# Kernel optimization log

Measured on AMD Instinct MI355X. Metric: run time of the kernel, lower is better.

## Reference

```python
import math
import jax, jax.numpy as jnp
import numpy as np

HEAD_DIM = 128
NUM_HEADS = 16
ROPE_BASE = 10000.0


def _rope_tables(seq_len, dim, dtype):
    inv_freq = 1.0 / (ROPE_BASE ** (jnp.arange(0, dim, 2, dtype=jnp.float32) / dim))
    t = jnp.arange(seq_len, dtype=jnp.float32)
    freqs = jnp.einsum('i,j->ij', t, inv_freq)          # [S, D/2]
    emb = jnp.concatenate([freqs, freqs], axis=-1)       # [S, D]
    return jnp.cos(emb).astype(dtype), jnp.sin(emb).astype(dtype)


def _rotate_half(x):
    x1, x2 = jnp.split(x, 2, axis=-1)
    return jnp.concatenate([-x2, x1], axis=-1)


def _apply_rope(x, cos, sin):
    # x: [B, S, H, D]; cos/sin: [S, D] broadcast over batch and heads
    return x * cos[None, :, None, :] + _rotate_half(x) * sin[None, :, None, :]


def setup_inputs() -> dict:
    key = jax.random.key(0)
    k1, k2, k3 = jax.random.split(key, 3)
    B, S, dim = 2, 2048, 2048
    out_dim = (NUM_HEADS + 2 * NUM_HEADS) * HEAD_DIM  # kvph=1 -> 3*H*D = 6144
    x = jax.random.normal(k1, (B, S, dim), dtype=jnp.float32)
    w_qkv = jax.random.normal(k2, (out_dim, dim), dtype=jnp.float32) * 0.02
    w_out = jax.random.normal(k3, (dim, NUM_HEADS * HEAD_DIM), dtype=jnp.float32) * 0.02
    return {"x": x, "w_qkv": w_qkv, "w_out": w_out}


def reference(x, w_qkv, w_out):
    B, S, _ = x.shape
    H, D = NUM_HEADS, HEAD_DIM
    qkv = jnp.einsum('bsd,od->bso', x, w_qkv)            # [B, S, 3*H*D]
    qkv = qkv.reshape(B, S, 3 * H, D)
    q = qkv[:, :, :H, :]                                 # [B, S, H, D]
    k = qkv[:, :, H:2 * H, :]
    v = qkv[:, :, 2 * H:, :]
    cos, sin = _rope_tables(S, D, x.dtype)
    q = _apply_rope(q, cos, sin)
    k = _apply_rope(k, cos, sin)
    scale = 1.0 / math.sqrt(D)
    logits = jnp.einsum('bqhd,bkhd->bhqk', q, k) * scale  # [B, H, S, S]
    attn = jax.nn.softmax(logits.astype(jnp.float32), axis=-1).astype(logits.dtype)
    out = jnp.einsum('bhqk,bkhd->bqhd', attn, v)          # [B, S, H, D]
    out = out.reshape(B, S, H * D)
    return jnp.einsum('bso,do->bsd', out, w_out)
```

## Files before the change

kernel.cpp:

```cpp
#include <hip/hip_runtime.h>
#include <math.h>
#include <stdint.h>

typedef unsigned short u16;
typedef unsigned int u32;
typedef float f32x4 __attribute__((ext_vector_type(4)));
typedef __bf16 bf16x8 __attribute__((ext_vector_type(8)));

typedef const __attribute__((address_space(1))) u32* gas1;
typedef __attribute__((address_space(3))) u32* las3;

#define B_ 2
#define S_ 2048
#define DM_ 2048
#define H_ 16
#define HD_ 128
#define NO_ 6144
#define M_ 4096

__device__ __forceinline__ u16 f2bf(float f) {
  u32 u = __float_as_uint(f);
  u32 r = (u + 0x7fffu + ((u >> 16) & 1u)) >> 16;
  return (u16)r;
}
__device__ __forceinline__ float bf2f(u16 h) {
  return __uint_as_float(((u32)h) << 16);
}

__global__ void prep_all(const float* __restrict__ x, const float* __restrict__ wqkv,
                         const float* __restrict__ wout, u16* __restrict__ xbf,
                         u16* __restrict__ wqkvb, u16* __restrict__ woutb,
                         float* __restrict__ ct, float* __restrict__ st) {
  const int C1 = (M_ * DM_) / 4, C2 = (NO_ * DM_) / 4, C3 = (DM_ * DM_) / 4;
  const int C4 = S_ * 64;
  const int total = C1 + C2 + C3 + C4;
  for (int i = blockIdx.x * blockDim.x + threadIdx.x; i < total;
       i += gridDim.x * blockDim.x) {
    if (i < C1 + C2 + C3) {
      const float* in;
      u16* out;
      int k;
      if (i < C1) {
        in = x; out = xbf; k = i;
      } else if (i < C1 + C2) {
        in = wqkv; out = wqkvb; k = i - C1;
      } else {
        in = wout; out = woutb; k = i - C1 - C2;
      }
      float4 v = *(const float4*)(in + (size_t)k * 4);
      ushort4 o;
      o.x = f2bf(v.x); o.y = f2bf(v.y); o.z = f2bf(v.z); o.w = f2bf(v.w);
      *(ushort4*)(out + (size_t)k * 4) = o;
    } else {
      int k = i - (C1 + C2 + C3);
      int s = k >> 6, j = k & 63;
      float inv = powf(10000.0f, -(float)j / 64.0f);
      float f = (float)s * inv;
      ct[k] = cosf(f);
      st[k] = sinf(f);
    }
  }
}

__global__ __launch_bounds__(512, 2) void gemm8_bt(const u16* __restrict__ A,
                                                   const u16* __restrict__ B,
                                                   u16* __restrict__ C,
                                                   int M, int N, int K, int ldc) {
  __shared__ u16 lds8[2][2][2][8192];
  const int t = threadIdx.x;
  const int w = t >> 6, l = t & 63, lr = l & 15, lg = l >> 4;
  const int wm = w >> 2, wn = w & 3;
  const int m0 = blockIdx.y * 256, n0 = blockIdx.x * 256;
  const int r0 = t >> 2;
  const int c = (t & 3) ^ ((t >> 3) & 3);
  const int swr = (lr >> 1) & 3;
  const u16* pA0 = A + (size_t)(m0 + r0) * K + c * 8;
  const u16* pB0 = B + (size_t)(n0 + r0) * K + c * 8;
  const size_t j1 = (size_t)128 * K;

  f32x4 acc[8][4] = {};
  bf16x8 af[8], bq[4];

  const int NT = K / 64, NI = NT / 2;

#define STG(T_, kh_, op_, buf_)                                                      \
  do {                                                                               \
    const u16* s_ = (op_ ? pB0 : pA0) + (T_) * 64 + (kh_) * 32;                      \
    u16* d_ = &lds8[buf_][op_][kh_][0] + w * 512;                                    \
    __builtin_amdgcn_global_load_lds((gas1)s_, (las3)d_, 16, 0, 0);                  \
    __builtin_amdgcn_global_load_lds((gas1)(s_ + j1), (las3)(d_ + 4096), 16, 0, 0);  \
  } while (0)

#define LDF(buf_, kh_)                                                            \
  do {                                                                            \
    const u16* a_ = &lds8[buf_][0][kh_][0];                                       \
    const u16* b_ = &lds8[buf_][1][kh_][0];                                       \
    _Pragma("unroll") for (int mi = 0; mi < 8; ++mi)                              \
        af[mi] = *(const bf16x8*)&a_[(wm * 128 + mi * 16 + lr) * 32 +             \
                                     ((lg ^ swr) * 8)];                           \
    _Pragma("unroll") for (int ni = 0; ni < 4; ++ni)                              \
        bq[ni] = *(const bf16x8*)&b_[(wn * 64 + ni * 16 + lr) * 32 +              \
                                     ((lg ^ swr) * 8)];                           \
  } while (0)

#define MFH(h_)                                                                \
  do {                                                                         \
    __builtin_amdgcn_s_setprio(1);                                             \
    _Pragma("unroll") for (int mi = 0; mi < 4; ++mi)                           \
        _Pragma("unroll") for (int ni = 0; ni < 4; ++ni)                       \
            acc[(h_) * 4 + mi][ni] = __builtin_amdgcn_mfma_f32_16x16x32_bf16(  \
                af[(h_) * 4 + mi], bq[ni], acc[(h_) * 4 + mi][ni], 0, 0, 0);   \
    __builtin_amdgcn_s_setprio(0);                                             \
  } while (0)

#define BAR() __builtin_amdgcn_s_barrier()
#define LGKM0() asm volatile("s_waitcnt lgkmcnt(0)" ::: "memory")
#define VM6() asm volatile("s_waitcnt vmcnt(6)" ::: "memory")

  STG(0, 0, 0, 0); STG(0, 0, 1, 0); STG(0, 1, 0, 0); STG(0, 1, 1, 0);
  STG(1, 0, 0, 1); STG(1, 0, 1, 1); STG(1, 1, 0, 1);
  VM6();
  BAR();

  for (int i = 0; i < NI; ++i) {
    const int T = 2 * i;
    const int Tp2 = (T + 2 < NT) ? T + 2 : NT - 1;
    const int Tp3 = (T + 3 < NT) ? T + 3 : NT - 1;
    LDF(0, 0);
    STG(T + 1, 1, 1, 1);
    BAR(); LGKM0(); MFH(0); BAR();
    STG(Tp2, 0, 0, 0);
    BAR(); MFH(1); BAR();
    LDF(0, 1);
    STG(Tp2, 0, 1, 0);
    BAR(); LGKM0(); MFH(0); BAR();
    STG(Tp2, 1, 0, 0);
    VM6(); BAR(); MFH(1); BAR();
    LDF(1, 0);
    STG(Tp2, 1, 1, 0);
    BAR(); LGKM0(); MFH(0); BAR();
    STG(Tp3, 0, 0, 1);
    BAR(); MFH(1); BAR();
    LDF(1, 1);
    STG(Tp3, 0, 1, 1);
    BAR(); LGKM0(); MFH(0); BAR();
    STG(Tp3, 1, 0, 1);
    VM6(); BAR(); MFH(1); BAR();
  }
  asm volatile("s_waitcnt vmcnt(0)" ::: "memory");
  BAR();

#pragma unroll
  for (int mi = 0; mi < 8; ++mi)
#pragma unroll
    for (int ni = 0; ni < 4; ++ni) {
      int row = m0 + wm * 128 + mi * 16 + lg * 4;
      int col = n0 + wn * 64 + ni * 16 + lr;
#pragma unroll
      for (int j = 0; j < 4; ++j)
        C[(size_t)(row + j) * ldc + col] = f2bf(acc[mi][ni][j]);
    }
#undef STG
#undef LDF
#undef MFH
#undef BAR
#undef LGKM0
#undef VM6
}

template <int OUT_BF16>
__global__ __launch_bounds__(256) void gemm_bt(const u16* __restrict__ A,
                                               const u16* __restrict__ B,
                                               void* __restrict__ Cv,
                                               int M, int N, int K, int ldc) {
  __shared__ u16 lA[128 * 32];
  __shared__ u16 lB[128 * 32];
  const int t = threadIdx.x;
  const int m0 = blockIdx.y * 128, n0 = blockIdx.x * 128;
  const int w = t >> 6, l = t & 63, lr = l & 15, lg = l >> 4;
  const int wm = (w >> 1) * 64, wn = (w & 1) * 64;
  f32x4 acc[4][4] = {};
  const int srow = t >> 2;
  const int scol = ((t & 3) ^ ((t >> 3) & 3)) * 8;
  const int swr = (lr >> 1) & 3;
  const u16* Ag = A + (size_t)(m0 + srow) * K + scol;
  const u16* Bg = B + (size_t)(n0 + srow) * K + scol;

  for (int k0 = 0; k0 < K; k0 += 32) {
    __syncthreads();
#pragma unroll
    for (int i = 0; i < 2; i++) {
      __builtin_amdgcn_global_load_lds((gas1)(Ag + (size_t)i * 64 * K + k0),
                                       (las3)(lA + (i * 256 + w * 64) * 8), 16, 0, 0);
      __builtin_amdgcn_global_load_lds((gas1)(Bg + (size_t)i * 64 * K + k0),
                                       (las3)(lB + (i * 256 + w * 64) * 8), 16, 0, 0);
    }
    __syncthreads();
    bf16x8 af[4], bfr[4];
#pragma unroll
    for (int mi = 0; mi < 4; mi++)
      af[mi] = *(const bf16x8*)&lA[(wm + mi * 16 + lr) * 32 + (lg ^ swr) * 8];
#pragma unroll
    for (int ni = 0; ni < 4; ni++)
      bfr[ni] = *(const bf16x8*)&lB[(wn + ni * 16 + lr) * 32 + (lg ^ swr) * 8];
#pragma unroll
    for (int mi = 0; mi < 4; mi++)
#pragma unroll
      for (int ni = 0; ni < 4; ni++)
        acc[mi][ni] =
            __builtin_amdgcn_mfma_f32_16x16x32_bf16(af[mi], bfr[ni], acc[mi][ni], 0, 0, 0);
  }

#pragma unroll
  for (int mi = 0; mi < 4; mi++)
#pragma unroll
    for (int ni = 0; ni < 4; ni++) {
      int row = m0 + wm + mi * 16 + lg * 4;
      int col = n0 + wn + ni * 16 + lr;
      if (OUT_BF16) {
        u16* C = (u16*)Cv;
#pragma unroll
        for (int j = 0; j < 4; j++) C[(size_t)(row + j) * ldc + col] = f2bf(acc[mi][ni][j]);
      } else {
        float* C = (float*)Cv;
#pragma unroll
        for (int j = 0; j < 4; j++) C[(size_t)(row + j) * ldc + col] = acc[mi][ni][j];
      }
    }
}

__global__ void rope_apply(u16* __restrict__ qkv, const float* __restrict__ ct,
                           const float* __restrict__ st) {
  int i = blockIdx.x * blockDim.x + threadIdx.x;
  int j = (i & 31) * 2;
  int hh = (i >> 5) & 31;
  int row = i >> 10;
  int s = row & (S_ - 1);
  int col = (hh < 16) ? hh * 128 : 2048 + (hh - 16) * 128;
  u16* p = qkv + (size_t)row * NO_ + col + j;
  u32 a = *(const u32*)&p[0];
  u32 bm = *(const u32*)&p[64];
  float2 cc = *(const float2*)&ct[(s << 6) + j];
  float2 ss = *(const float2*)&st[(s << 6) + j];
  float e10 = bf2f((u16)a), e11 = bf2f((u16)(a >> 16));
  float e20 = bf2f((u16)bm), e21 = bf2f((u16)(bm >> 16));
  float o10 = e10 * cc.x - e20 * ss.x;
  float o11 = e11 * cc.y - e21 * ss.y;
  float o20 = e20 * cc.x + e10 * ss.x;
  float o21 = e21 * cc.y + e11 * ss.y;
  if (hh < 16) {
    const float kq = 0.08838834764831845f * 1.4426950408889634f;
    o10 *= kq; o11 *= kq; o20 *= kq; o21 *= kq;
  }
  *(u32*)&p[0] = (u32)f2bf(o10) | ((u32)f2bf(o11) << 16);
  *(u32*)&p[64] = (u32)f2bf(o20) | ((u32)f2bf(o21) << 16);
}

__global__ __launch_bounds__(256) void transpose_v(const u16* __restrict__ qkv,
                                                   u16* __restrict__ vt) {
  __shared__ u16 lds[128 * 64];
  const int bh = blockIdx.y;
  const int b = bh >> 4, h = bh & 15;
  const int s0 = blockIdx.x * 64;
  const int t = threadIdx.x;
  union { uint4 v; u16 e[8]; } uu;
#pragma unroll
  for (int i = 0; i < 4; i++) {
    int s = i * 16 + (t >> 4);
    int dc = (t & 15) * 8;
    uu.v = *(const uint4*)(qkv + (size_t)(b * S_ + s0 + s) * NO_ + 4096 + h * 128 + dc);
#pragma unroll
    for (int q = 0; q < 8; q++) {
      int d = dc + q;
      lds[d * 64 + (s ^ (((d >> 3) & 7) << 3))] = uu.e[q];
    }
  }
  __syncthreads();
#pragma unroll
  for (int i = 0; i < 4; i++) {
    int d = i * 32 + (t >> 3);
    int sc = (t & 7) * 8;
    uint4 v = *(const uint4*)&lds[d * 64 + (sc ^ (((d >> 3) & 7) << 3))];
    *(uint4*)(vt + (size_t)(bh * 128 + d) * S_ + s0 + sc) = v;
  }
}

__global__ __launch_bounds__(256, 2) void flash_attn(const u16* __restrict__ qkv,
                                                     const u16* __restrict__ vt,
                                                     u16* __restrict__ ao) {
  __shared__ u16 lK[2][64 * 128];
  __shared__ u16 lV[2][128 * 64];
  __shared__ u16 lP[4][2][16 * 64];
  const int t = threadIdx.x;
  const int w = t >> 6, l = t & 63, lr = l & 15, lg = l >> 4;
  const int bid = blockIdx.y * gridDim.x + blockIdx.x;
  const int xcd = bid & 7, v = bid >> 3;
  const int bh = xcd + 8 * (v >> 4);
  const int q0 = (v & 15) * 128;
  const int b = bh >> 4, h = bh & 15;

  bf16x8 qf[2][4];
#pragma unroll
  for (int g = 0; g < 2; g++) {
    const u16* Qg = qkv + (size_t)(b * S_ + q0 + w * 32 + g * 16 + lr) * NO_ + h * 128;
#pragma unroll
    for (int c = 0; c < 4; c++) qf[g][c] = *(const bf16x8*)(Qg + c * 32 + lg * 8);
  }

  f32x4 acc[2][8] = {};
  float l_run[2] = {0.f, 0.f};

  const u16* ksrc[4];
  const u16* vsrc[4];
#pragma unroll
  for (int q = 0; q < 4; q++) {
    int rt = w * 16 + q * 4 + (l >> 4);
    int ck = (l & 15) ^ (rt & 15);
    ksrc[q] = qkv + (size_t)(b * S_ + rt) * NO_ + 2048 + h * 128 + ck * 8;
    int d = w * 32 + q * 8 + (l >> 3);
    int cv = (l & 7) ^ (d & 7);
    vsrc[q] = vt + (size_t)(bh * 128 + d) * S_ + cv * 8;
  }

#pragma unroll
  for (int q = 0; q < 4; q++) {
    __builtin_amdgcn_global_load_lds((gas1)ksrc[q],
                                     (las3)(lK[0] + (w * 16 + q * 4) * 128), 16, 0, 0);
    __builtin_amdgcn_global_load_lds((gas1)vsrc[q],
                                     (las3)(lV[0] + (w * 32 + q * 8) * 64), 16, 0, 0);
    ksrc[q] += (size_t)64 * NO_;
    vsrc[q] += 64;
  }
  __syncthreads();

  const int NT = S_ / 64;
  for (int kt = 0; kt < NT; kt++) {
    const int cur = kt & 1;
    if (kt + 1 < NT) {
#pragma unroll
      for (int q = 0; q < 4; q++) {
        __builtin_amdgcn_global_load_lds((gas1)ksrc[q],
                                         (las3)(lK[cur ^ 1] + (w * 16 + q * 4) * 128), 16, 0, 0);
        __builtin_amdgcn_global_load_lds((gas1)vsrc[q],
                                         (las3)(lV[cur ^ 1] + (w * 32 + q * 8) * 64), 16, 0, 0);
        ksrc[q] += (size_t)64 * NO_;
        vsrc[q] += 64;
      }
    }

    f32x4 sc[2][4];
#pragma unroll
    for (int g = 0; g < 2; g++)
#pragma unroll
      for (int cb = 0; cb < 4; cb++) sc[g][cb] = (f32x4){0.f, 0.f, 0.f, 0.f};
    __builtin_amdgcn_s_setprio(1);
#pragma unroll
    for (int cb = 0; cb < 4; cb++) {
      int r = cb * 16 + lr;
#pragma unroll
      for (int c = 0; c < 4; c++) {
        bf16x8 kf = *(const bf16x8*)&lK[cur][r * 128 + ((c * 32 + lg * 8) ^ ((r & 15) << 3))];
        sc[0][cb] = __builtin_amdgcn_mfma_f32_16x16x32_bf16(kf, qf[0][c], sc[0][cb], 0, 0, 0);
        sc[1][cb] = __builtin_amdgcn_mfma_f32_16x16x32_bf16(kf, qf[1][c], sc[1][cb], 0, 0, 0);
      }
    }
    __builtin_amdgcn_s_setprio(0);

#pragma unroll
    for (int g = 0; g < 2; g++) {
      float ps = 0.f;
#pragma unroll
      for (int cb = 0; cb < 4; cb++)
#pragma unroll
        for (int j = 0; j < 4; j++) {
          float p = exp2f(sc[g][cb][j]);
          sc[g][cb][j] = p;
          ps += p;
        }
      l_run[g] += ps;
    }

#pragma unroll
    for (int g = 0; g < 2; g++) {
      u16* lPw = lP[w][g];
#pragma unroll
      for (int cb = 0; cb < 4; cb++) {
        u32 p01, p23;
        asm("v_cvt_pk_bf16_f32 %0, %1, %2" : "=v"(p01) : "v"(sc[g][cb][0]), "v"(sc[g][cb][1]));
        asm("v_cvt_pk_bf16_f32 %0, %1, %2" : "=v"(p23) : "v"(sc[g][cb][2]), "v"(sc[g][cb][3]));
        uint2 pk;
        pk.x = p01;
        pk.y = p23;
        *(uint2*)&lPw[lr * 64 + ((cb * 16 + lg * 4) ^ ((lr & 7) << 3))] = pk;
      }
    }

    __builtin_amdgcn_s_setprio(1);
#pragma unroll
    for (int c2 = 0; c2 < 2; c2++) {
      bf16x8 pf0 = *(const bf16x8*)&lP[w][0][lr * 64 + ((c2 * 32 + lg * 8) ^ ((lr & 7) << 3))];
      bf16x8 pf1 = *(const bf16x8*)&lP[w][1][lr * 64 + ((c2 * 32 + lg * 8) ^ ((lr & 7) << 3))];
#pragma unroll
      for (int nb = 0; nb < 8; nb++) {
        int r = nb * 16 + lr;
        bf16x8 vf = *(const bf16x8*)&lV[cur][r * 64 + ((c2 * 32 + lg * 8) ^ ((r & 7) << 3))];
        acc[0][nb] = __builtin_amdgcn_mfma_f32_16x16x32_bf16(pf0, vf, acc[0][nb], 0, 0, 0);
        acc[1][nb] = __builtin_amdgcn_mfma_f32_16x16x32_bf16(pf1, vf, acc[1][nb], 0, 0, 0);
      }
    }
    __builtin_amdgcn_s_setprio(0);

    __syncthreads();
  }

#pragma unroll
  for (int g = 0; g < 2; g++) {
    float lsum = l_run[g];
    lsum += __shfl_xor(lsum, 16);
    lsum += __shfl_xor(lsum, 32);
    float linv[4];
#pragma unroll
    for (int j = 0; j < 4; j++) linv[j] = 1.0f / __shfl(lsum, lg * 4 + j);
#pragma unroll
    for (int nb = 0; nb < 8; nb++)
#pragma unroll
      for (int j = 0; j < 4; j++) {
        int qrow = q0 + w * 32 + g * 16 + lg * 4 + j;
        ao[(size_t)(b * S_ + qrow) * 2048 + h * 128 + nb * 16 + lr] =
            f2bf(acc[g][nb][j] * linv[j]);
      }
  }
}

extern "C" void kernel_launch(void* const* d_in, const int* in_sizes, int n_in,
                              void* d_out, int out_size, void* d_ws, size_t ws_size,
                              hipStream_t stream) {
  const float* x = (const float*)d_in[0];
  const float* wqkv = (const float*)d_in[1];
  const float* wout = (const float*)d_in[2];
  float* out = (float*)d_out;

  char* ws = (char*)d_ws;
  u16* xbf = (u16*)(ws);
  u16* wqkvb = (u16*)(ws + ((size_t)16 << 20));
  u16* woutb = (u16*)(ws + ((size_t)40 << 20));
  u16* qkv = (u16*)(ws + ((size_t)48 << 20));
  u16* vtb = (u16*)(ws + ((size_t)96 << 20));
  float* ct = (float*)(ws + ((size_t)112 << 20));
  float* st = (float*)(ws + ((size_t)112 << 20) + ((size_t)1 << 19));
  u16* aout = xbf;

  prep_all<<<2048, 256, 0, stream>>>(x, wqkv, wout, xbf, wqkvb, woutb, ct, st);
  gemm8_bt<<<dim3(16, 16), 512, 0, stream>>>(xbf, wqkvb, qkv, M_, 4096, DM_, NO_);
  gemm_bt<1><<<dim3(16, 32), 256, 0, stream>>>(
      xbf, wqkvb + (size_t)4096 * DM_, qkv + 4096, M_, 2048, DM_, NO_);
  rope_apply<<<(M_ * 32 * 32) / 256, 256, 0, stream>>>(qkv, ct, st);
  transpose_v<<<dim3(S_ / 64, B_ * H_), 256, 0, stream>>>(qkv, vtb);
  flash_attn<<<dim3(16, 32), 256, 0, stream>>>(qkv, vtb, aout);
  gemm_bt<0><<<dim3(DM_ / 128, M_ / 128), 256, 0, stream>>>(aout, woutb, out, M_, DM_, DM_,
                                                            DM_);
}
```

Baseline: 305.8 us.

## Fuse RoPE into QK GEMM epilogue and V transpose into V GEMM

Applies rotary embedding and the Q scale directly in the QK GEMM epilogue. Each wave swaps its accumulator tile with its partner wave (the other half of the head dim) through LDS, and reads transposed cos/sin tables. The V projection GEMM now writes V transposed through an LDS staging tile. This removes the separate rope_apply and transpose_v kernels along with their extra global reads and writes of qkv. In exchange, the epilogues carry extra LDS traffic, a barrier and strided table loads, and the partner pairing relies on the tile layout mapping half-dims to adjacent waves.

```diff
diff --git a/kernel.cpp b/kernel.cpp
--- a/kernel.cpp
+++ b/kernel.cpp
@@ -30,9 +30,9 @@
 __global__ void prep_all(const float* __restrict__ x, const float* __restrict__ wqkv,
                          const float* __restrict__ wout, u16* __restrict__ xbf,
                          u16* __restrict__ wqkvb, u16* __restrict__ woutb,
-                         float* __restrict__ ct, float* __restrict__ st) {
+                         float* __restrict__ ctT, float* __restrict__ stT) {
   const int C1 = (M_ * DM_) / 4, C2 = (NO_ * DM_) / 4, C3 = (DM_ * DM_) / 4;
-  const int C4 = S_ * 64;
+  const int C4 = 64 * S_;
   const int total = C1 + C2 + C3 + C4;
   for (int i = blockIdx.x * blockDim.x + threadIdx.x; i < total;
        i += gridDim.x * blockDim.x) {
@@ -53,11 +53,11 @@
       *(ushort4*)(out + (size_t)k * 4) = o;
     } else {
       int k = i - (C1 + C2 + C3);
-      int s = k >> 6, j = k & 63;
+      int j = k >> 11, s = k & 2047;
       float inv = powf(10000.0f, -(float)j / 64.0f);
       float f = (float)s * inv;
-      ct[k] = cosf(f);
-      st[k] = sinf(f);
+      ctT[k] = cosf(f);
+      stT[k] = sinf(f);
     }
   }
 }
@@ -65,7 +65,9 @@
 __global__ __launch_bounds__(512, 2) void gemm8_bt(const u16* __restrict__ A,
                                                    const u16* __restrict__ B,
                                                    u16* __restrict__ C,
-                                                   int M, int N, int K, int ldc) {
+                                                   int M, int N, int K, int ldc,
+                                                   const float* __restrict__ ctT,
+                                                   const float* __restrict__ stT) {
   __shared__ u16 lds8[2][2][2][8192];
   const int t = threadIdx.x;
   const int w = t >> 6, l = t & 63, lr = l & 15, lg = l >> 4;
@@ -150,16 +152,49 @@
   asm volatile("s_waitcnt vmcnt(0)" ::: "memory");
   BAR();
 
+  u16* xb = (u16*)lds8;
 #pragma unroll
   for (int mi = 0; mi < 8; ++mi)
 #pragma unroll
     for (int ni = 0; ni < 4; ++ni) {
-      int row = m0 + wm * 128 + mi * 16 + lg * 4;
+      ushort4 pk;
+      pk.x = f2bf(acc[mi][ni][0]);
+      pk.y = f2bf(acc[mi][ni][1]);
+      pk.z = f2bf(acc[mi][ni][2]);
+      pk.w = f2bf(acc[mi][ni][3]);
+      int li = (l * 4) ^ ((l >> 4) << 3);
+      *(ushort4*)&xb[(w * 32 + mi * 4 + ni) * 256 + li] = pk;
+    }
+  __syncthreads();
+  const int wp = w ^ 1;
+  const int pos = w & 1;
+  const bool isQ = (n0 < 2048);
+  const float kq = 0.08838834764831845f * 1.4426950408889634f;
+#pragma unroll
+  for (int mi = 0; mi < 8; ++mi) {
+    int row = m0 + wm * 128 + mi * 16 + lg * 4;
+    int s0 = row & (S_ - 1);
+#pragma unroll
+    for (int ni = 0; ni < 4; ++ni) {
+      int li = (l * 4) ^ ((l >> 4) << 3);
+      ushort4 pp = *(const ushort4*)&xb[(wp * 32 + mi * 4 + ni) * 256 + li];
+      int j0 = ni * 16 + lr;
+      float4 c4 = *(const float4*)&ctT[j0 * S_ + s0];
+      float4 s4 = *(const float4*)&stT[j0 * S_ + s0];
       int col = n0 + wn * 64 + ni * 16 + lr;
-#pragma unroll
-      for (int j = 0; j < 4; ++j)
-        C[(size_t)(row + j) * ldc + col] = f2bf(acc[mi][ni][j]);
-    }
+      const u16 pe[4] = {pp.x, pp.y, pp.z, pp.w};
+      const float cc[4] = {c4.x, c4.y, c4.z, c4.w};
+      const float sv[4] = {s4.x, s4.y, s4.z, s4.w};
+#pragma unroll
+      for (int j = 0; j < 4; ++j) {
+        float own = acc[mi][ni][j];
+        float part = bf2f(pe[j]);
+        float o = pos ? own * cc[j] + part * sv[j] : own * cc[j] - part * sv[j];
+        if (isQ) o *= kq;
+        C[(size_t)(row + j) * ldc + col] = f2bf(o);
+      }
+    }
+  }
 #undef STG
 #undef LDF
 #undef MFH
@@ -168,7 +203,7 @@
 #undef VM6
 }
 
-template <int OUT_BF16>
+template <int MODE>
 __global__ __launch_bounds__(256) void gemm_bt(const u16* __restrict__ A,
                                                const u16* __restrict__ B,
                                                void* __restrict__ Cv,
@@ -211,77 +246,52 @@
             __builtin_amdgcn_mfma_f32_16x16x32_bf16(af[mi], bfr[ni], acc[mi][ni], 0, 0, 0);
   }
 
-#pragma unroll
-  for (int mi = 0; mi < 4; mi++)
-#pragma unroll
-    for (int ni = 0; ni < 4; ni++) {
-      int row = m0 + wm + mi * 16 + lg * 4;
-      int col = n0 + wn + ni * 16 + lr;
-      if (OUT_BF16) {
-        u16* C = (u16*)Cv;
-#pragma unroll
-        for (int j = 0; j < 4; j++) C[(size_t)(row + j) * ldc + col] = f2bf(acc[mi][ni][j]);
-      } else {
-        float* C = (float*)Cv;
-#pragma unroll
-        for (int j = 0; j < 4; j++) C[(size_t)(row + j) * ldc + col] = acc[mi][ni][j];
-      }
-    }
-}
-
-__global__ void rope_apply(u16* __restrict__ qkv, const float* __restrict__ ct,
-                           const float* __restrict__ st) {
-  int i = blockIdx.x * blockDim.x + threadIdx.x;
-  int j = (i & 31) * 2;
-  int hh = (i >> 5) & 31;
-  int row = i >> 10;
-  int s = row & (S_ - 1);
-  int col = (hh < 16) ? hh * 128 : 2048 + (hh - 16) * 128;
-  u16* p = qkv + (size_t)row * NO_ + col + j;
-  u32 a = *(const u32*)&p[0];
-  u32 bm = *(const u32*)&p[64];
-  float2 cc = *(const float2*)&ct[(s << 6) + j];
-  float2 ss = *(const float2*)&st[(s << 6) + j];
-  float e10 = bf2f((u16)a), e11 = bf2f((u16)(a >> 16));
-  float e20 = bf2f((u16)bm), e21 = bf2f((u16)(bm >> 16));
-  float o10 = e10 * cc.x - e20 * ss.x;
-  float o11 = e11 * cc.y - e21 * ss.y;
-  float o20 = e20 * cc.x + e10 * ss.x;
-  float o21 = e21 * cc.y + e11 * ss.y;
-  if (hh < 16) {
-    const float kq = 0.08838834764831845f * 1.4426950408889634f;
-    o10 *= kq; o11 *= kq; o20 *= kq; o21 *= kq;
-  }
-  *(u32*)&p[0] = (u32)f2bf(o10) | ((u32)f2bf(o11) << 16);
-  *(u32*)&p[64] = (u32)f2bf(o20) | ((u32)f2bf(o21) << 16);
-}
-
-__global__ __launch_bounds__(256) void transpose_v(const u16* __restrict__ qkv,
-                                                   u16* __restrict__ vt) {
-  __shared__ u16 lds[128 * 64];
-  const int bh = blockIdx.y;
-  const int b = bh >> 4, h = bh & 15;
-  const int s0 = blockIdx.x * 64;
-  const int t = threadIdx.x;
-  union { uint4 v; u16 e[8]; } uu;
-#pragma unroll
-  for (int i = 0; i < 4; i++) {
-    int s = i * 16 + (t >> 4);
-    int dc = (t & 15) * 8;
-    uu.v = *(const uint4*)(qkv + (size_t)(b * S_ + s0 + s) * NO_ + 4096 + h * 128 + dc);
-#pragma unroll
-    for (int q = 0; q < 8; q++) {
-      int d = dc + q;
-      lds[d * 64 + (s ^ (((d >> 3) & 7) << 3))] = uu.e[q];
-    }
-  }
-  __syncthreads();
-#pragma unroll
-  for (int i = 0; i < 4; i++) {
-    int d = i * 32 + (t >> 3);
-    int sc = (t & 7) * 8;
-    uint4 v = *(const uint4*)&lds[d * 64 + (sc ^ (((d >> 3) & 7) << 3))];
-    *(uint4*)(vt + (size_t)(bh * 128 + d) * S_ + s0 + sc) = v;
+  if constexpr (MODE == 2) {
+    __shared__ u16 tbuf[128 * 128];
+#pragma unroll
+    for (int mi = 0; mi < 4; mi++)
+#pragma unroll
+      for (int ni = 0; ni < 4; ni++) {
+        int r0 = wm + mi * 16 + lg * 4;
+        int d = wn + ni * 16 + lr;
+        ushort4 pk;
+        pk.x = f2bf(acc[mi][ni][0]);
+        pk.y = f2bf(acc[mi][ni][1]);
+        pk.z = f2bf(acc[mi][ni][2]);
+        pk.w = f2bf(acc[mi][ni][3]);
+        *(ushort4*)&tbuf[d * 128 + (r0 ^ ((d & 7) << 3))] = pk;
+      }
+    __syncthreads();
+    const int h = n0 >> 7;
+    const int b = m0 >> 11;
+    const int s0 = m0 & (S_ - 1);
+    u16* vt = (u16*)Cv;
+#pragma unroll
+    for (int i = 0; i < 8; i++) {
+      int d = i * 16 + (t >> 4);
+      int sc = (t & 15) * 8;
+      uint4 vv = *(const uint4*)&tbuf[d * 128 + (sc ^ ((d & 7) << 3))];
+      *(uint4*)&vt[(size_t)((b * 16 + h) * 128 + d) * S_ + s0 + sc] = vv;
+    }
+  } else {
+#pragma unroll
+    for (int mi = 0; mi < 4; mi++)
+#pragma unroll
+      for (int ni = 0; ni < 4; ni++) {
+        int row = m0 + wm + mi * 16 + lg * 4;
+        int col = n0 + wn + ni * 16 + lr;
+        if (MODE == 1) {
+          u16* C = (u16*)Cv;
+#pragma unroll
+          for (int j = 0; j < 4; j++)
+            C[(size_t)(row + j) * ldc + col] = f2bf(acc[mi][ni][j]);
+        } else {
+          float* C = (float*)Cv;
+#pragma unroll
+          for (int j = 0; j < 4; j++)
+            C[(size_t)(row + j) * ldc + col] = acc[mi][ni][j];
+        }
+      }
   }
 }
 
@@ -446,16 +456,15 @@
   u16* woutb = (u16*)(ws + ((size_t)40 << 20));
   u16* qkv = (u16*)(ws + ((size_t)48 << 20));
   u16* vtb = (u16*)(ws + ((size_t)96 << 20));
-  float* ct = (float*)(ws + ((size_t)112 << 20));
-  float* st = (float*)(ws + ((size_t)112 << 20) + ((size_t)1 << 19));
+  float* ctT = (float*)(ws + ((size_t)112 << 20));
+  float* stT = (float*)(ws + ((size_t)112 << 20) + ((size_t)1 << 19));
   u16* aout = xbf;
 
-  prep_all<<<2048, 256, 0, stream>>>(x, wqkv, wout, xbf, wqkvb, woutb, ct, st);
-  gemm8_bt<<<dim3(16, 16), 512, 0, stream>>>(xbf, wqkvb, qkv, M_, 4096, DM_, NO_);
-  gemm_bt<1><<<dim3(16, 32), 256, 0, stream>>>(
-      xbf, wqkvb + (size_t)4096 * DM_, qkv + 4096, M_, 2048, DM_, NO_);
-  rope_apply<<<(M_ * 32 * 32) / 256, 256, 0, stream>>>(qkv, ct, st);
-  transpose_v<<<dim3(S_ / 64, B_ * H_), 256, 0, stream>>>(qkv, vtb);
+  prep_all<<<2048, 256, 0, stream>>>(x, wqkv, wout, xbf, wqkvb, woutb, ctT, stT);
+  gemm8_bt<<<dim3(16, 16), 512, 0, stream>>>(xbf, wqkvb, qkv, M_, 4096, DM_, NO_, ctT,
+                                             stT);
+  gemm_bt<2><<<dim3(16, 32), 256, 0, stream>>>(xbf, wqkvb + (size_t)4096 * DM_, vtb, M_,
+                                               2048, DM_, 0);
   flash_attn<<<dim3(16, 32), 256, 0, stream>>>(qkv, vtb, aout);
   gemm_bt<0><<<dim3(DM_ / 128, M_ / 128), 256, 0, stream>>>(aout, woutb, out, M_, DM_, DM_,
                                                             DM_);
```

Measured after the change: 300.5 us, median of 2. Within noise of the previous version (-1.7%).
